# Kernel optimization log

Hardware: AMD Instinct MI355X
Metric: run time of the kernel (lower is better)

## Reference

```python
import jax, jax.numpy as jnp
import numpy as np
import math

B, T, D, NH, HD = 2, 1024, 768, 12, 64
V, L, E, CAP_F, H = 50257, 2, 8, 1.25, 2048
AUX_W, Z_W, THETA, EPS = 0.01, 0.001, 10000.0, 1e-5
N = B * T
CAP = int(math.ceil(N / E * CAP_F))  # 320


def setup_inputs():
    key = jax.random.key(0)
    ks = jax.random.split(key, 8)
    s = 0.02
    return dict(
        idx=jax.random.randint(ks[0], (B, T), 0, V),
        wte=jax.random.normal(ks[1], (V, D), jnp.float32) * s,
        wqkv=jax.random.normal(ks[2], (L, D, 3 * D), jnp.float32) * s,
        q_norm_w=jnp.ones((L, D), jnp.float32),
        k_norm_w=jnp.ones((L, D), jnp.float32),
        o_proj=jax.random.normal(ks[3], (L, D, D), jnp.float32) * s,
        ffn_norm_w=jnp.ones((L, D), jnp.float32),
        gate_w=jax.random.normal(ks[4], (L, D, E), jnp.float32) * s,
        w13=jax.random.normal(ks[5], (L, E, D, 2 * H), jnp.float32) * s,
        w2=jax.random.normal(ks[6], (L, E, H, D), jnp.float32) * s,
        ln_f_w=jnp.ones((D,), jnp.float32),
    )


def rmsnorm(x, w):
    return x * jax.lax.rsqrt(jnp.mean(x * x, axis=-1, keepdims=True) + EPS) * w


def rope(x, cos, sin):
    # x: (B, nh, T, HD) viewed as complex pairs on last dim
    xr = x.reshape(*x.shape[:-1], HD // 2, 2)
    x0, x1 = xr[..., 0], xr[..., 1]
    out = jnp.stack([x0 * cos - x1 * sin, x0 * sin + x1 * cos], axis=-1)
    return out.reshape(x.shape)


def moe(x, gate_w, w13, w2):
    # x: (B, T, D) -> Switch MoE (k=1) with capacity CAP and token drops
    x_flat = x.reshape(N, D).astype(jnp.float32)
    logits = x_flat @ gate_w  # (N, E) fp32
    probs = jax.nn.softmax(logits, axis=-1)
    top = jnp.argmax(logits, axis=-1)  # (N,)
    prob_mass = probs.mean(axis=0)
    fraction = jax.nn.one_hot(top, E, dtype=jnp.float32).mean(axis=0)
    balance_loss = jnp.sum(prob_mass * fraction) * AUX_W * E
    z = jax.nn.logsumexp(logits, axis=-1)
    z_loss = jnp.mean(z * z) * Z_W
    aux = balance_loss + z_loss

    sort_idx = jnp.argsort(top)  # stable
    sorted_assign = top[sort_idx]
    counts = jnp.bincount(sorted_assign, length=E)
    offsets = jnp.concatenate([jnp.zeros((1,), counts.dtype), jnp.cumsum(counts)])[:E]
    rank = jnp.arange(N) - offsets[sorted_assign]  # position within expert segment
    keep = rank < CAP
    x_perm = x_flat[sort_idx]
    slot = jnp.where(keep, rank, CAP)  # dropped -> overflow slot
    buf = jnp.zeros((E, CAP + 1, D), jnp.float32).at[sorted_assign, slot].set(x_perm)
    xb = buf[:, :CAP]  # (E, CAP, D)
    gu = jnp.einsum('ecd,edh->ech', xb, w13)  # (E, CAP, 2H)
    g, u = jnp.split(gu, 2, axis=-1)
    y = jnp.einsum('ech,ehd->ecd', jax.nn.silu(g) * u, w2)  # (E, CAP, D)
    out_perm = y[sorted_assign, jnp.minimum(rank, CAP - 1)] * keep[:, None]
    out_flat = jnp.zeros((N, D), jnp.float32).at[sort_idx].set(out_perm)
    return out_flat.reshape(B, T, D), aux, top.reshape(B, T), keep[jnp.argsort(sort_idx)].reshape(B, T)


def forward(idx, wte, wqkv, q_norm_w, k_norm_w, o_proj, ffn_norm_w, gate_w, w13, w2, ln_f_w):
    x = wte[idx]  # (B, T, D)
    freqs = 1.0 / (THETA ** (jnp.arange(0, HD, 2, dtype=jnp.float32) / HD))
    ang = jnp.outer(jnp.arange(T, dtype=jnp.float32), freqs)  # (T, HD//2)
    cos, sin = jnp.cos(ang)[None, None], jnp.sin(ang)[None, None]
    mask = jnp.where(jnp.tril(jnp.ones((T, T), bool)), 0.0, -jnp.inf)
    aux_total = jnp.float32(0.0)
    for l in range(L):
        qkv = x @ wqkv[l]
        q, k, v = jnp.split(qkv, 3, axis=-1)
        q = rmsnorm(q, q_norm_w[l])
        k = rmsnorm(k, k_norm_w[l])
        q = q.reshape(B, T, NH, HD).transpose(0, 2, 1, 3)
        k = k.reshape(B, T, NH, HD).transpose(0, 2, 1, 3)
        v = v.reshape(B, T, NH, HD).transpose(0, 2, 1, 3)
        q, k = rope(q, cos, sin), rope(k, cos, sin)
        scores = jnp.einsum('bhqd,bhkd->bhqk', q, k) / math.sqrt(HD) + mask
        attn = jax.nn.softmax(scores, axis=-1)
        y = jnp.einsum('bhqk,bhkd->bhqd', attn, v).transpose(0, 2, 1, 3).reshape(B, T, D)
        h = x + y @ o_proj[l]
        ffn_in = rmsnorm(h, ffn_norm_w[l])
        moe_out, aux, _, _ = moe(ffn_in, gate_w[l], w13[l], w2[l])
        aux_total = aux_total + aux
        x = h + moe_out
    x = rmsnorm(x, ln_f_w)
    logits = x @ wte.T  # tied lm_head
    return logits, aux_total


def reference(idx, wte, wqkv, q_norm_w, k_norm_w, o_proj, ffn_norm_w, gate_w, w13, w2, ln_f_w):
    return forward(idx, wte, wqkv, q_norm_w, k_norm_w, o_proj, ffn_norm_w, gate_w, w13, w2, ln_f_w)
```

## Files before the change

### kernel.cpp

```cpp
#include <hip/hip_runtime.h>

typedef __attribute__((ext_vector_type(8))) _Float16 half8;
typedef __attribute__((ext_vector_type(4))) float f32x4;

constexpr int Bc = 2, Tc = 1024, Dc = 768, NHc = 12, HDc = 64;
constexpr int Vc = 50257, Lc = 2, Ec = 8, Hc = 2048;
constexpr int Ntok = Bc * Tc;
constexpr int CAPc = 320, CAPPc = 384;
constexpr long long LOGITS_N = (long long)Bc * Tc * Vc;

typedef const __attribute__((address_space(1))) unsigned int* gas_t;
typedef __attribute__((address_space(3))) unsigned int* las_t;
__device__ __forceinline__ void gload16(const void* g, void* l) {
  __builtin_amdgcn_global_load_lds((gas_t)g, (las_t)l, 16, 0, 0);
}

__device__ __forceinline__ void splitf16(float a, unsigned short& h, unsigned short& l) {
  _Float16 hh = (_Float16)a;
  _Float16 ll = (_Float16)(a - (float)hh);
  h = __builtin_bit_cast(unsigned short, hh);
  l = __builtin_bit_cast(unsigned short, ll);
}
__device__ __forceinline__ unsigned short f16o(float a) {
  _Float16 hh = (_Float16)a;
  return __builtin_bit_cast(unsigned short, hh);
}


__global__ void zero_small(float* psum, float* z2) {
  int t = threadIdx.x;
  if (t < Lc * Ec) psum[t] = 0.f;
  if (t < Lc) z2[t] = 0.f;
}

__global__ void embed_k(const int* __restrict__ idx, const float* __restrict__ wte,
                        float* __restrict__ x, unsigned short* __restrict__ x16) {
  int n = blockIdx.x;
  long long v = idx[n];
  const float4* src = (const float4*)(wte + v * 768);
  float4* dst = (float4*)(x + (long long)n * 768);
  int t = threadIdx.x;
  if (t < 192) {
    float4 val = src[t];
    dst[t] = val;
    ushort4 h, l;
    splitf16(val.x, h.x, l.x); splitf16(val.y, h.y, l.y);
    splitf16(val.z, h.z, l.z); splitf16(val.w, h.w, l.w);
    unsigned short* d = x16 + (long long)n * 1536 + t * 4;
    *(ushort4*)d = h;
    *(ushort4*)(d + 768) = l;
  }
}

__global__ void f2h4(const float* __restrict__ in, unsigned short* __restrict__ out,
                     long long n4) {
  long long i = (long long)blockIdx.x * 256 + threadIdx.x;
  if (i >= n4) return;
  float4 v = ((const float4*)in)[i];
  ushort4 o;
  o.x = f16o(v.x); o.y = f16o(v.y); o.z = f16o(v.z); o.w = f16o(v.w);
  ((ushort4*)out)[i] = o;
}

template <int SP>
__global__ void __launch_bounds__(256) split2_wT(const float* __restrict__ src,
    unsigned short* __restrict__ dst, int K, int N, long long sS, long long sD) {
  __shared__ float t[32][33];
  int z = blockIdx.z;
  src += (long long)z * sS;
  dst += (long long)z * sD;
  int n0 = blockIdx.x * 32, k0 = blockIdx.y * 32;
  int tid = threadIdx.x;
  int r = tid >> 3, c4 = (tid & 7) * 4;
  float4 v = *(const float4*)(src + (long long)(k0 + r) * N + n0 + c4);
  t[r][c4 + 0] = v.x; t[r][c4 + 1] = v.y; t[r][c4 + 2] = v.z; t[r][c4 + 3] = v.w;
  __syncthreads();
  int n = tid >> 3, kq = (tid & 7) * 4;
  ushort4 h, l;
  splitf16(t[kq + 0][n], h.x, l.x);
  splitf16(t[kq + 1][n], h.y, l.y);
  splitf16(t[kq + 2][n], h.z, l.z);
  splitf16(t[kq + 3][n], h.w, l.w);
  const int lda = SP ? 2 * K : K;
  unsigned short* d = dst + (long long)(n0 + n) * lda + k0 + kq;
  *(ushort4*)d = h;
  if (SP) *(ushort4*)(d + K) = l;
}

__global__ void __launch_bounds__(256) rmsnorm_k(const float* in, int istride,
                                                 float* outp, int ostride,
                                                 const float* w) {
  long long n = blockIdx.x;
  const float* xr = in + n * istride;
  float* yr = outp + n * ostride;
  int tid = threadIdx.x;
  float s = 0.f;
  for (int i = tid; i < 768; i += 256) { float v = xr[i]; s += v * v; }
  #pragma unroll
  for (int o = 32; o; o >>= 1) s += __shfl_down(s, o);
  __shared__ float red[4];
  __shared__ float bs;
  if ((tid & 63) == 0) red[tid >> 6] = s;
  __syncthreads();
  if (tid == 0) bs = rsqrtf((red[0] + red[1] + red[2] + red[3]) / 768.0f + 1e-5f);
  __syncthreads();
  float sc = bs;
  for (int i = tid; i < 768; i += 256) yr[i] = xr[i] * sc * w[i];
}

__global__ void __launch_bounds__(256) rmsnorm_h(const float* in,
                                                 unsigned short* outp, const float* w) {
  long long n = blockIdx.x;
  const float* xr = in + n * 768;
  unsigned short* yr = outp + n * 768;
  int tid = threadIdx.x;
  float s = 0.f;
  for (int i = tid; i < 768; i += 256) { float v = xr[i]; s += v * v; }
  #pragma unroll
  for (int o = 32; o; o >>= 1) s += __shfl_down(s, o);
  __shared__ float red[4];
  __shared__ float bs;
  if ((tid & 63) == 0) red[tid >> 6] = s;
  __syncthreads();
  if (tid == 0) bs = rsqrtf((red[0] + red[1] + red[2] + red[3]) / 768.0f + 1e-5f);
  __syncthreads();
  float sc = bs;
  for (int i = tid; i < 768; i += 256) yr[i] = f16o(xr[i] * sc * w[i]);
}

__global__ void __launch_bounds__(256) qk_rope(const float* __restrict__ qkv,
    const float* __restrict__ qnw, const float* __restrict__ knw,
    unsigned short* __restrict__ qr, unsigned short* __restrict__ kr,
    unsigned short* __restrict__ vr) {
  int n = blockIdx.x;
  int t = n & 1023, b = n >> 10;
  const float* row = qkv + (long long)n * 2304;
  int tid = threadIdx.x;
  float sq = 0.f, sk = 0.f;
  for (int i = tid; i < 768; i += 256) {
    float q = row[i]; sq += q * q;
    float k = row[768 + i]; sk += k * k;
  }
  #pragma unroll
  for (int o = 32; o; o >>= 1) { sq += __shfl_down(sq, o); sk += __shfl_down(sk, o); }
  __shared__ float redq[4], redk[4];
  __shared__ float bq, bk;
  if ((tid & 63) == 0) { redq[tid >> 6] = sq; redk[tid >> 6] = sk; }
  __syncthreads();
  if (tid == 0) {
    bq = rsqrtf((redq[0] + redq[1] + redq[2] + redq[3]) / 768.0f + 1e-5f);
    bk = rsqrtf((redk[0] + redk[1] + redk[2] + redk[3]) / 768.0f + 1e-5f);
  }
  __syncthreads();
  float nq = bq, nk = bk;
  for (int i = tid; i < 384; i += 256) {
    int hh = i >> 5, j = i & 31;
    int c = hh * 64 + 2 * j;
    float ang = (float)t * powf(10000.0f, -((float)j * (1.0f / 32.0f)));
    float cs = cosf(ang), sn = sinf(ang);
    int z = b * 12 + hh;
    long long qb = ((long long)z * 1024 + t) * 128 + 2 * j;
    unsigned short h0, l0, h1, l1;
    float q0 = row[c] * nq * qnw[c], q1 = row[c + 1] * nq * qnw[c + 1];
    splitf16(q0 * cs - q1 * sn, h0, l0);
    splitf16(q0 * sn + q1 * cs, h1, l1);
    *(unsigned int*)&qr[qb] = (unsigned)h0 | ((unsigned)h1 << 16);
    *(unsigned int*)&qr[qb + 64] = (unsigned)l0 | ((unsigned)l1 << 16);
    float k0 = row[768 + c] * nk * knw[c], k1 = row[768 + c + 1] * nk * knw[c + 1];
    splitf16(k0 * cs - k1 * sn, h0, l0);
    splitf16(k0 * sn + k1 * cs, h1, l1);
    *(unsigned int*)&kr[qb] = (unsigned)h0 | ((unsigned)h1 << 16);
    *(unsigned int*)&kr[qb + 64] = (unsigned)l0 | ((unsigned)l1 << 16);
    splitf16(row[1536 + c], h0, l0);
    splitf16(row[1536 + c + 1], h1, l1);
    long long vb = ((long long)z * 64 + 2 * j) * 2048 + t;
    vr[vb] = h0; vr[vb + 1024] = l0;
    vr[vb + 2048] = h1; vr[vb + 3072] = l1;
  }
}

__global__ void __launch_bounds__(256) flash_attn(
    const unsigned short* __restrict__ qr, const unsigned short* __restrict__ kr,
    const unsigned short* __restrict__ vr, unsigned short* __restrict__ yout) {
  __shared__ __align__(16) unsigned short Ph[4][16][72];
  __shared__ __align__(16) unsigned short Pl[4][16][72];
  int bid = blockIdx.x;
  int z = bid >> 4;
  int qt = 15 - (bid & 15);
  int b = z / 12, h = z % 12;
  int q0 = qt * 64;
  int wave = threadIdx.x >> 6, lane = threadIdx.x & 63;
  int lr = lane & 15, lg = lane >> 4;
  int qw = q0 + wave * 16;
  half8 af[2][2];
  const unsigned short* qbase = qr + ((long long)z * 1024 + qw + lr) * 128;
  #pragma unroll
  for (int ks = 0; ks < 2; ++ks)
    #pragma unroll
    for (int p = 0; p < 2; ++p)
      af[ks][p] = *(const half8*)(qbase + p * 64 + ks * 32 + lg * 8);
  f32x4 accy[4];
  #pragma unroll
  for (int df = 0; df < 4; ++df) accy[df] = (f32x4){0.f, 0.f, 0.f, 0.f};
  float mrun[4] = {-3.4e38f, -3.4e38f, -3.4e38f, -3.4e38f};
  float srun[4] = {0.f, 0.f, 0.f, 0.f};
  for (int kt = 0; kt <= qt; ++kt) {
    int kv0 = kt * 64;
    f32x4 s[4];
    #pragma unroll
    for (int nf = 0; nf < 4; ++nf) s[nf] = (f32x4){0.f, 0.f, 0.f, 0.f};
    const unsigned short* kbase = kr + ((long long)z * 1024 + kv0 + lr) * 128;
    #pragma unroll
    for (int nf = 0; nf < 4; ++nf) {
      const unsigned short* kb = kbase + nf * 16 * 128;
      #pragma unroll
      for (int ks = 0; ks < 2; ++ks) {
        half8 bh = *(const half8*)(kb + ks * 32 + lg * 8);
        half8 bl = *(const half8*)(kb + 64 + ks * 32 + lg * 8);
        s[nf] = __builtin_amdgcn_mfma_f32_16x16x32_f16(af[ks][0], bh, s[nf], 0, 0, 0);
        s[nf] = __builtin_amdgcn_mfma_f32_16x16x32_f16(af[ks][1], bh, s[nf], 0, 0, 0);
        s[nf] = __builtin_amdgcn_mfma_f32_16x16x32_f16(af[ks][0], bl, s[nf], 0, 0, 0);
      }
    }
    bool diag = (kt == qt);
    #pragma unroll
    for (int nf = 0; nf < 4; ++nf)
      #pragma unroll
      for (int j = 0; j < 4; ++j) {
        float v = s[nf][j] * 0.125f;
        if (diag && (nf * 16 + lr > wave * 16 + lg * 4 + j)) v = -1e30f;
        s[nf][j] = v;
      }
    #pragma unroll
    for (int j = 0; j < 4; ++j) {
      float tm = fmaxf(fmaxf(s[0][j], s[1][j]), fmaxf(s[2][j], s[3][j]));
      #pragma unroll
      for (int o = 1; o < 16; o <<= 1) tm = fmaxf(tm, __shfl_xor(tm, o));
      float mnew = fmaxf(mrun[j], tm);
      float sc = expf(mrun[j] - mnew);
      float ts = 0.f;
      #pragma unroll
      for (int nf = 0; nf < 4; ++nf) {
        float p = expf(s[nf][j] - mnew);
        ts += p;
        unsigned short ph, pl;
        splitf16(p, ph, pl);
        Ph[wave][lg * 4 + j][nf * 16 + lr] = ph;
        Pl[wave][lg * 4 + j][nf * 16 + lr] = pl;
      }
      #pragma unroll
      for (int o = 1; o < 16; o <<= 1) ts += __shfl_xor(ts, o);
      srun[j] = srun[j] * sc + ts;
      mrun[j] = mnew;
      #pragma unroll
      for (int df = 0; df < 4; ++df) accy[df][j] *= sc;
    }
    #pragma unroll
    for (int ks2 = 0; ks2 < 2; ++ks2) {
      half8 aph = *(const half8*)&Ph[wave][lr][ks2 * 32 + lg * 8];
      half8 apl = *(const half8*)&Pl[wave][lr][ks2 * 32 + lg * 8];
      #pragma unroll
      for (int df = 0; df < 4; ++df) {
        const unsigned short* vb =
            vr + ((long long)z * 64 + df * 16 + lr) * 2048 + kv0 + ks2 * 32 + lg * 8;
        half8 bvh = *(const half8*)vb;
        half8 bvl = *(const half8*)(vb + 1024);
        accy[df] = __builtin_amdgcn_mfma_f32_16x16x32_f16(aph, bvh, accy[df], 0, 0, 0);
        accy[df] = __builtin_amdgcn_mfma_f32_16x16x32_f16(apl, bvh, accy[df], 0, 0, 0);
        accy[df] = __builtin_amdgcn_mfma_f32_16x16x32_f16(aph, bvl, accy[df], 0, 0, 0);
      }
    }
  }
  float inv[4];
  #pragma unroll
  for (int j = 0; j < 4; ++j) inv[j] = 1.0f / srun[j];
  #pragma unroll
  for (int df = 0; df < 4; ++df)
    #pragma unroll
    for (int j = 0; j < 4; ++j) {
      long long tok = (long long)b * 1024 + qw + lg * 4 + j;
      int col = h * 64 + df * 16 + lr;
      unsigned short hh, ll;
      splitf16(accy[df][j] * inv[j], hh, ll);
      yout[tok * 1536 + col] = hh;
      yout[tok * 1536 + 768 + col] = ll;
    }
}

__global__ void __launch_bounds__(256) gate_k(const float* __restrict__ xin,
    const float* __restrict__ gw, int* __restrict__ top,
    float* __restrict__ psum, float* __restrict__ z2) {
  __shared__ float gws[768 * 8];
  __shared__ float pacc[8];
  __shared__ float zacc;
  int tid = threadIdx.x;
  for (int i = tid; i < 768 * 8 / 4; i += 256) ((float4*)gws)[i] = ((const float4*)gw)[i];
  if (tid < 8) pacc[tid] = 0.f;
  if (tid == 0) zacc = 0.f;
  __syncthreads();
  int n = blockIdx.x * 256 + tid;
  const float4* xr4 = (const float4*)(xin + (long long)n * 768);
  float l[8] = {0, 0, 0, 0, 0, 0, 0, 0};
  for (int d4 = 0; d4 < 192; ++d4) {
    float4 xv = xr4[d4];
    const float* g = &gws[d4 * 32];
    #pragma unroll
    for (int e = 0; e < 8; ++e)
      l[e] += xv.x * g[e] + xv.y * g[8 + e] + xv.z * g[16 + e] + xv.w * g[24 + e];
  }
  float mx = l[0]; int bi = 0;
  #pragma unroll
  for (int e = 1; e < 8; ++e) if (l[e] > mx) { mx = l[e]; bi = e; }
  float p[8]; float se = 0.f;
  #pragma unroll
  for (int e = 0; e < 8; ++e) { p[e] = expf(l[e] - mx); se += p[e]; }
  float z = mx + logf(se);
  top[n] = bi;
  #pragma unroll
  for (int e = 0; e < 8; ++e) atomicAdd(&pacc[e], p[e] / se);
  atomicAdd(&zacc, z * z);
  __syncthreads();
  if (tid < 8) atomicAdd(&psum[tid], pacc[tid]);
  if (tid == 0) atomicAdd(z2, zacc);
}

__global__ void route_scan(const int* __restrict__ top, int* __restrict__ rank,
                           int* __restrict__ cnt) {
  int lane = threadIdx.x;
  int c[8] = {0, 0, 0, 0, 0, 0, 0, 0};
  unsigned long long below = (1ull << lane) - 1ull;
  for (int s = 0; s < Ntok / 64; ++s) {
    int n = s * 64 + lane;
    int e = top[n];
    int r = 0;
    #pragma unroll
    for (int q = 0; q < 8; ++q) {
      unsigned long long m = __ballot(e == q);
      if (e == q) r = c[q] + __popcll(m & below);
      c[q] += __popcll(m);
    }
    rank[n] = r;
  }
  #pragma unroll
  for (int q = 0; q < 8; ++q) if (lane == q) cnt[q] = c[q];
}

template <int SP>
__global__ void scatter_xb(const float* __restrict__ xin, const int* __restrict__ top,
                           const int* __restrict__ rank, unsigned short* __restrict__ xb) {
  int n = blockIdx.x;
  int r = rank[n];
  if (r >= CAPc) return;
  int e = top[n];
  int t = threadIdx.x;
  if (t >= 192) return;
  float4 v = ((const float4*)(xin + (long long)n * 768))[t];
  ushort4 h, l;
  splitf16(v.x, h.x, l.x); splitf16(v.y, h.y, l.y);
  splitf16(v.z, h.z, l.z); splitf16(v.w, h.w, l.w);
  const int lda = SP ? 1536 : 768;
  unsigned short* dst = xb + ((long long)e * CAPPc + r) * lda + t * 4;
  *(ushort4*)dst = h;
  if (SP) *(ushort4*)(dst + 768) = l;
}

template <int SP>
__global__ void __launch_bounds__(256) silu_k(const float* __restrict__ gu,
                                              unsigned short* __restrict__ act) {
  long long i = (long long)blockIdx.x * 256 + threadIdx.x;
  long long row = i >> 11;
  int h = (int)(i & 2047);
  float g = gu[row * 4096 + h];
  float u = gu[row * 4096 + 2048 + h];
  float a = g / (1.f + expf(-g)) * u;
  if (SP) {
    unsigned short hh, ll;
    splitf16(a, hh, ll);
    act[row * 4096 + h] = hh;
    act[row * 4096 + 2048 + h] = ll;
  } else {
    act[row * 2048 + h] = f16o(a);
  }
}

__global__ void gather_add(const float* __restrict__ h, const float* __restrict__ yexp,
                           const int* __restrict__ top, const int* __restrict__ rank,
                           float* __restrict__ xo, unsigned short* __restrict__ x16) {
  int n = blockIdx.x;
  int r = rank[n], e = top[n];
  bool kept = r < CAPc;
  int rc = kept ? r : (CAPc - 1);
  const float4* hs = (const float4*)(h + (long long)n * 768);
  const float4* ys = (const float4*)(yexp + ((long long)e * CAPPc + rc) * 768);
  float4* dst = (float4*)(xo + (long long)n * 768);
  int t = threadIdx.x;
  if (t < 192) {
    float4 v = hs[t];
    if (kept) { float4 y = ys[t]; v.x += y.x; v.y += y.y; v.z += y.z; v.w += y.w; }
    dst[t] = v;
    ushort4 hh, ll;
    splitf16(v.x, hh.x, ll.x); splitf16(v.y, hh.y, ll.y);
    splitf16(v.z, hh.z, ll.z); splitf16(v.w, hh.w, ll.w);
    unsigned short* d = x16 + (long long)n * 1536 + t * 4;
    *(ushort4*)d = hh;
    *(ushort4*)(d + 768) = ll;
  }
}

__global__ void aux_fin(const float* __restrict__ psum, const int* __restrict__ cnt,
                        const float* __restrict__ z2, float* __restrict__ outp) {
  if (threadIdx.x == 0) {
    float aux = 0.f;
    for (int l = 0; l < Lc; ++l) {
      float bl = 0.f;
      for (int e = 0; e < 8; ++e)
        bl += (psum[l * 8 + e] * (1.0f / 2048.0f)) * ((float)cnt[l * 8 + e] * (1.0f / 2048.0f));
      aux += bl * (0.01f * 8.0f) + (z2[l] * (1.0f / 2048.0f)) * 0.001f;
    }
    outp[0] = aux;
  }
}

template <int BN, int SPLIT, int ADD, int NTAIL>
__global__ void __launch_bounds__(256) gemm_h(
    const unsigned short* __restrict__ A, const unsigned short* __restrict__ Bt,
    float* __restrict__ C, const float* __restrict__ Add,
    int M, int N, int K, int ldc, int gx, int gy,
    long long sA, long long sB, int zdiv, long long sC1, long long sC2) {
  constexpr int FN = (BN == 128) ? 4 : 2;
  constexpr int APL = 128 * 32;
  constexpr int BPL = BN * 32;
  constexpr int BUF = 2 * APL + 2 * BPL;
  __shared__ __align__(16) unsigned short lds[2][BUF];
  int tot = gridDim.x;
  int lin = blockIdx.x;
  if ((tot & 7) == 0) lin = (lin & 7) * (tot >> 3) + (lin >> 3);
  int pz = lin / (gx * gy);
  int r2 = lin - pz * (gx * gy);
  const int m0 = (r2 % gx) * 128, n0 = (r2 / gx) * BN;
  A += (long long)pz * sA;
  Bt += (long long)pz * sB;
  const long long co = (long long)(pz / zdiv) * sC1 + (long long)(pz % zdiv) * sC2;
  const int lda = SPLIT ? 2 * K : K;
  const int NS = SPLIT ? K / 32 : K / 64;
  const int tid = threadIdx.x;
  const int lane = tid & 63, wave = tid >> 6;
  const int wm = (BN == 128) ? (wave >> 1) : (wave & 1);
  const int wn = (BN == 128) ? (wave & 1) : (wave >> 1);
  const int srow = tid >> 2, scol = (tid & 3) * 8;
  const unsigned short* Ar = A + (long long)(m0 + srow) * lda + scol;
  int br0 = n0 + srow;
  if (NTAIL) br0 = min(br0, N - 1);
  const unsigned short* Br = Bt + (long long)br0 * lda + scol;
  int br1 = n0 + srow + 64;
  if (NTAIL) br1 = min(br1, N - 1);
  const unsigned short* Br2 = Bt + (long long)br1 * lda + scol;

  auto STAGE = [&](int buf, int s) {
    const int kh = SPLIT ? s * 32 : s * 64;
    const int kl = SPLIT ? K + s * 32 : s * 64 + 32;
    unsigned short* L = lds[buf];
    gload16(Ar + kh, &L[wave * 512]);
    gload16(Ar + (long long)64 * lda + kh, &L[2048 + wave * 512]);
    gload16(Ar + kl, &L[APL + wave * 512]);
    gload16(Ar + (long long)64 * lda + kl, &L[APL + 2048 + wave * 512]);
    gload16(Br + kh, &L[2 * APL + wave * 512]);
    gload16(Br + kl, &L[2 * APL + BPL + wave * 512]);
    if (BN == 128) {
      gload16(Br2 + kh, &L[2 * APL + 2048 + wave * 512]);
      gload16(Br2 + kl, &L[2 * APL + BPL + 2048 + wave * 512]);
    }
  };

  f32x4 acc[4][FN];
  #pragma unroll
  for (int m = 0; m < 4; ++m)
    #pragma unroll
    for (int n = 0; n < FN; ++n) acc[m][n] = (f32x4){0.f, 0.f, 0.f, 0.f};

  STAGE(0, 0);
  int cur = 0;
  for (int s = 0; s < NS; ++s) {
    if (s + 1 < NS) {
      STAGE(cur ^ 1, s + 1);
      if constexpr (BN == 128)
        asm volatile("s_waitcnt vmcnt(8)" ::: "memory");
      else
        asm volatile("s_waitcnt vmcnt(6)" ::: "memory");
    } else {
      asm volatile("s_waitcnt vmcnt(0)" ::: "memory");
    }
    __builtin_amdgcn_sched_barrier(0);
    __builtin_amdgcn_s_barrier();
    const unsigned short* L = lds[cur];
    half8 bfh[FN], bfl[FN];
    #pragma unroll
    for (int n = 0; n < FN; ++n) {
      int bo = (wn * (FN * 16) + n * 16 + (lane & 15)) * 32 + (lane >> 4) * 8;
      bfh[n] = *(const half8*)&L[2 * APL + bo];
      bfl[n] = *(const half8*)&L[2 * APL + BPL + bo];
    }
    __builtin_amdgcn_s_setprio(1);
    #pragma unroll
    for (int m = 0; m < 4; ++m) {
      int ao = (wm * 64 + m * 16 + (lane & 15)) * 32 + (lane >> 4) * 8;
      half8 afh = *(const half8*)&L[ao];
      half8 afl = *(const half8*)&L[APL + ao];
      #pragma unroll
      for (int n = 0; n < FN; ++n) {
        acc[m][n] = __builtin_amdgcn_mfma_f32_16x16x32_f16(afh, bfh[n], acc[m][n], 0, 0, 0);
        if (SPLIT) {
          acc[m][n] = __builtin_amdgcn_mfma_f32_16x16x32_f16(afl, bfh[n], acc[m][n], 0, 0, 0);
          acc[m][n] = __builtin_amdgcn_mfma_f32_16x16x32_f16(afh, bfl[n], acc[m][n], 0, 0, 0);
        } else {
          acc[m][n] = __builtin_amdgcn_mfma_f32_16x16x32_f16(afl, bfl[n], acc[m][n], 0, 0, 0);
        }
      }
    }
    __builtin_amdgcn_s_setprio(0);
    __builtin_amdgcn_sched_barrier(0);
    __builtin_amdgcn_s_barrier();
    cur ^= 1;
  }
  #pragma unroll
  for (int m = 0; m < 4; ++m)
    #pragma unroll
    for (int n = 0; n < FN; ++n) {
      int col = n0 + wn * (FN * 16) + n * 16 + (lane & 15);
      if (!NTAIL || col < N) {
        #pragma unroll
        for (int j = 0; j < 4; ++j) {
          long long row = m0 + wm * 64 + m * 16 + (lane >> 4) * 4 + j;
          long long o = co + row * ldc + col;
          float v = acc[m][n][j];
          if (ADD) v += Add[o];
          C[o] = v;
        }
      }
    }
}


extern "C" void kernel_launch(void* const* d_in, const int* in_sizes, int n_in,
                              void* d_out, int out_size, void* d_ws, size_t ws_size,
                              hipStream_t stream) {
  (void)in_sizes; (void)n_in; (void)out_size; (void)ws_size;
  const int*   idx   = (const int*)d_in[0];
  const float* wte   = (const float*)d_in[1];
  const float* wqkv  = (const float*)d_in[2];
  const float* qnw   = (const float*)d_in[3];
  const float* knw   = (const float*)d_in[4];
  const float* oproj = (const float*)d_in[5];
  const float* ffnw  = (const float*)d_in[6];
  const float* gatew = (const float*)d_in[7];
  const float* w13   = (const float*)d_in[8];
  const float* w2p   = (const float*)d_in[9];
  const float* lnf   = (const float*)d_in[10];
  float* out = (float*)d_out;

  char* base = (char*)d_ws;
  size_t off = 0;
  auto alloc = [&](size_t bytes) -> char* {
    off = (off + 255) & ~(size_t)255;
    char* p = base + off; off += bytes; return p;
  };
  float* x     = (float*)alloc((size_t)Ntok * 768 * 4);
  float* qkv   = (float*)alloc((size_t)Ntok * 2304 * 4);
  float* hbuf  = (float*)alloc((size_t)Ntok * 768 * 4);
  float* ffn   = (float*)alloc((size_t)Ntok * 768 * 4);
  unsigned short* x16   = (unsigned short*)alloc((size_t)Ntok * 1536 * 2);
  unsigned short* yfl16 = (unsigned short*)alloc((size_t)Ntok * 1536 * 2);
  unsigned short* qr16  = (unsigned short*)alloc((size_t)24 * 1024 * 128 * 2);
  unsigned short* kr16  = (unsigned short*)alloc((size_t)24 * 1024 * 128 * 2);
  unsigned short* vr16  = (unsigned short*)alloc((size_t)24 * 64 * 2048 * 2);
  unsigned short* xb16  = (unsigned short*)alloc((size_t)Ec * CAPPc * 1536 * 2);
  unsigned short* wo16  = (unsigned short*)alloc((size_t)768 * 1536 * 2);
  unsigned short* xf16  = (unsigned short*)alloc((size_t)Ntok * 768 * 2);
  char* spb = alloc((size_t)24 * 1024 * 1024 * 4);
  float* gu   = (float*)spb;
  float* yexp = (float*)spb;
  unsigned short* act16 = (unsigned short*)(spb + 50331648);
  unsigned short* wq16  = (unsigned short*)(spb + 75497472);
  unsigned short* w13_16 = (unsigned short*)alloc((size_t)Ec * 4096 * 1536 * 2);
  unsigned short* wt16   = w13_16;
  unsigned short* w2_16  = (unsigned short*)alloc((size_t)Ec * 768 * 4096 * 2);
  int* top    = (int*)alloc(Ntok * 4);
  int* rankb  = (int*)alloc(Ntok * 4);
  int* cnt    = (int*)alloc(Lc * Ec * 4);
  float* psum = (float*)alloc(Lc * Ec * 4);
  float* z2   = (float*)alloc(Lc * 4);

  zero_small<<<1, 64, 0, stream>>>(psum, z2);
  embed_k<<<Ntok, 192, 0, stream>>>(idx, wte, x, x16);

  for (int l = 0; l < Lc; ++l) {
    split2_wT<1><<<dim3(72, 24, 1), 256, 0, stream>>>(wqkv + (size_t)l * 768 * 2304, wq16,
                                                      768, 2304, 0, 0);
    split2_wT<1><<<dim3(24, 24, 1), 256, 0, stream>>>(oproj + (size_t)l * 768 * 768, wo16,
                                                      768, 768, 0, 0);
    if (l == 0) {
      split2_wT<1><<<dim3(128, 24, 8), 256, 0, stream>>>(w13, w13_16,
          768, 4096, (long long)768 * 4096, (long long)4096 * 1536);
      split2_wT<1><<<dim3(24, 64, 8), 256, 0, stream>>>(w2p, w2_16,
          2048, 768, (long long)2048 * 768, (long long)768 * 4096);
    } else {
      split2_wT<0><<<dim3(128, 24, 8), 256, 0, stream>>>(w13 + (size_t)Ec * 768 * 4096, w13_16,
          768, 4096, (long long)768 * 4096, (long long)4096 * 768);
      split2_wT<0><<<dim3(24, 64, 8), 256, 0, stream>>>(w2p + (size_t)Ec * 2048 * 768, w2_16,
          2048, 768, (long long)2048 * 768, (long long)768 * 2048);
    }
    gemm_h<128, 1, 0, 0><<<288, 256, 0, stream>>>(
        x16, wq16, qkv, nullptr, 2048, 2304, 768, 2304, 16, 18, 0, 0, 1, 0, 0);
    qk_rope<<<Ntok, 256, 0, stream>>>(qkv, qnw + l * 768, knw + l * 768, qr16, kr16, vr16);
    flash_attn<<<384, 256, 0, stream>>>(qr16, kr16, vr16, yfl16);
    gemm_h<64, 1, 1, 0><<<192, 256, 0, stream>>>(
        yfl16, wo16, hbuf, x, 2048, 768, 768, 768, 16, 12, 0, 0, 1, 0, 0);
    rmsnorm_k<<<Ntok, 256, 0, stream>>>(hbuf, 768, ffn, 768, ffnw + l * 768);
    gate_k<<<Ntok / 256, 256, 0, stream>>>(ffn, gatew + (size_t)l * 768 * 8, top,
                                           psum + l * 8, z2 + l);
    route_scan<<<1, 64, 0, stream>>>(top, rankb, cnt + l * 8);
    if (l == 0) {
      scatter_xb<1><<<Ntok, 192, 0, stream>>>(ffn, top, rankb, xb16);
      gemm_h<128, 1, 0, 0><<<768, 256, 0, stream>>>(
          xb16, w13_16, gu, nullptr, 384, 4096, 768, 4096, 3, 32,
          (long long)384 * 1536, (long long)4096 * 1536, 1, (long long)384 * 4096, 0);
      silu_k<1><<<(Ec * CAPPc * Hc) / 256, 256, 0, stream>>>(gu, act16);
      gemm_h<64, 1, 0, 0><<<288, 256, 0, stream>>>(
          act16, w2_16, yexp, nullptr, 384, 768, 2048, 768, 3, 12,
          (long long)384 * 4096, (long long)768 * 4096, 1, (long long)384 * 768, 0);
    } else {
      scatter_xb<0><<<Ntok, 192, 0, stream>>>(ffn, top, rankb, xb16);
      gemm_h<128, 0, 0, 0><<<768, 256, 0, stream>>>(
          xb16, w13_16, gu, nullptr, 384, 4096, 768, 4096, 3, 32,
          (long long)384 * 768, (long long)4096 * 768, 1, (long long)384 * 4096, 0);
      silu_k<0><<<(Ec * CAPPc * Hc) / 256, 256, 0, stream>>>(gu, act16);
      gemm_h<64, 0, 0, 0><<<288, 256, 0, stream>>>(
          act16, w2_16, yexp, nullptr, 384, 768, 2048, 768, 3, 12,
          (long long)384 * 2048, (long long)768 * 2048, 1, (long long)384 * 768, 0);
    }
    gather_add<<<Ntok, 192, 0, stream>>>(hbuf, yexp, top, rankb, x, x16);
  }

  rmsnorm_h<<<Ntok, 256, 0, stream>>>(x, xf16, lnf);
  f2h4<<<(int)(((long long)Vc * 768 / 4 + 255) / 256), 256, 0, stream>>>(
      wte, wt16, (long long)Vc * 768 / 4);
  gemm_h<128, 0, 0, 1><<<6288, 256, 0, stream>>>(
      xf16, wt16, out, nullptr, 2048, Vc, 768, Vc, 16, 393, 0, 0, 1, 0, 0);
  aux_fin<<<1, 64, 0, stream>>>(psum, cnt, z2, out + LOGITS_N);
}
```

Measured before the change: 1.286 ms.

## Add dedicated triple-buffered 256x128 MFMA GEMM for the tied lm_head logits

Replaces the generic gemm_h call for the final vocabulary projection with a specialized kernel. It uses 256x128 tiles, 512 threads, three LDS stages fed by async global-to-LDS loads, an XOR-swizzled LDS layout and an XCD-aware block remap. The aim is to overlap loads with MFMA work and reuse more data per tile in the largest GEMM. The cost is higher LDS use per block (about 144 KB), which limits occupancy. Row indices outside N are clamped, so the wasted loads in the tail tile stay in bounds.

```diff
diff --git a/kernel.cpp b/kernel.cpp
--- a/kernel.cpp
+++ b/kernel.cpp
@@ -540,6 +540,102 @@
     }
 }
 
+__global__ void __launch_bounds__(512) gemm_logits(
+    const unsigned short* __restrict__ A, const unsigned short* __restrict__ Bt,
+    float* __restrict__ C, int M, int N, int K, int ldc, int gx) {
+  constexpr int BUFS = 24576;
+  constexpr int BOFF = 16384;
+  __shared__ __align__(16) unsigned short lds[3 * BUFS];
+  int tot = gridDim.x;
+  int lin = blockIdx.x;
+  if ((tot & 7) == 0) lin = (lin & 7) * (tot >> 3) + (lin >> 3);
+  const int m0 = (lin % gx) * 256, n0 = (lin / gx) * 128;
+  const int tid = threadIdx.x;
+  const int lane = tid & 63;
+  const int wm = (tid >> 6) >> 1, wn = (tid >> 6) & 1;
+  const int NS = K / 64;
+
+  auto STAGE = [&](int buf, int t) {
+    const int k0 = t * 64;
+    unsigned short* L = lds + buf * BUFS;
+    #pragma unroll
+    for (int i = 0; i < 4; ++i) {
+      int idx = tid + i * 512;
+      int row = idx >> 3, blk = idx & 7;
+      gload16(A + (long long)(m0 + row) * K + k0 + ((blk ^ (row & 7)) << 3),
+              L + idx * 8);
+    }
+    #pragma unroll
+    for (int i = 0; i < 2; ++i) {
+      int idx = tid + i * 512;
+      int row = idx >> 3, blk = idx & 7;
+      int br = min(n0 + row, N - 1);
+      gload16(Bt + (long long)br * K + k0 + ((blk ^ (row & 7)) << 3),
+              L + BOFF + idx * 8);
+    }
+  };
+
+  f32x4 acc[4][4];
+  #pragma unroll
+  for (int mf = 0; mf < 4; ++mf)
+    #pragma unroll
+    for (int nf = 0; nf < 4; ++nf) acc[mf][nf] = (f32x4){0.f, 0.f, 0.f, 0.f};
+
+  STAGE(0, 0); STAGE(1, 1); STAGE(2, 2);
+  for (int s = 0; s < NS; ++s) {
+    if (s + 3 <= NS)      asm volatile("s_waitcnt vmcnt(12)" ::: "memory");
+    else if (s + 2 <= NS) asm volatile("s_waitcnt vmcnt(6)" ::: "memory");
+    else                  asm volatile("s_waitcnt vmcnt(0)" ::: "memory");
+    __builtin_amdgcn_sched_barrier(0);
+    __builtin_amdgcn_s_barrier();
+    const unsigned short* L = lds + (s % 3) * BUFS;
+    half8 a[4][2], b[4][2];
+    #pragma unroll
+    for (int mf = 0; mf < 4; ++mf)
+      #pragma unroll
+      for (int ks = 0; ks < 2; ++ks) {
+        int row = wm * 64 + mf * 16 + (lane & 15);
+        int blk = (ks * 4 + (lane >> 4)) ^ (row & 7);
+        a[mf][ks] = *(const half8*)(L + row * 64 + blk * 8);
+      }
+    #pragma unroll
+    for (int nf = 0; nf < 4; ++nf)
+      #pragma unroll
+      for (int ks = 0; ks < 2; ++ks) {
+        int row = wn * 64 + nf * 16 + (lane & 15);
+        int blk = (ks * 4 + (lane >> 4)) ^ (row & 7);
+        b[nf][ks] = *(const half8*)(L + BOFF + row * 64 + blk * 8);
+      }
+    asm volatile("s_waitcnt lgkmcnt(0)" ::: "memory");
+    __builtin_amdgcn_sched_barrier(0);
+    __builtin_amdgcn_s_barrier();
+    if (s + 3 < NS) STAGE((s + 3) % 3, s + 3);
+    __builtin_amdgcn_s_setprio(1);
+    #pragma unroll
+    for (int ks = 0; ks < 2; ++ks)
+      #pragma unroll
+      for (int mf = 0; mf < 4; ++mf)
+        #pragma unroll
+        for (int nf = 0; nf < 4; ++nf)
+          acc[mf][nf] = __builtin_amdgcn_mfma_f32_16x16x32_f16(a[mf][ks], b[nf][ks],
+                                                               acc[mf][nf], 0, 0, 0);
+    __builtin_amdgcn_s_setprio(0);
+  }
+  #pragma unroll
+  for (int mf = 0; mf < 4; ++mf)
+    #pragma unroll
+    for (int nf = 0; nf < 4; ++nf) {
+      int col = n0 + wn * 64 + nf * 16 + (lane & 15);
+      if (col < N) {
+        #pragma unroll
+        for (int j = 0; j < 4; ++j) {
+          long long row = m0 + wm * 64 + mf * 16 + (lane >> 4) * 4 + j;
+          C[row * (long long)ldc + col] = acc[mf][nf][j];
+        }
+      }
+    }
+}
+
 
 extern "C" void kernel_launch(void* const* d_in, const int* in_sizes, int n_in,
                               void* d_out, int out_size, void* d_ws, size_t ws_size,
@@ -644,7 +740,6 @@
   rmsnorm_h<<<Ntok, 256, 0, stream>>>(x, xf16, lnf);
   f2h4<<<(int)(((long long)Vc * 768 / 4 + 255) / 256), 256, 0, stream>>>(
       wte, wt16, (long long)Vc * 768 / 4);
-  gemm_h<128, 0, 0, 1><<<6288, 256, 0, stream>>>(
-      xf16, wt16, out, nullptr, 2048, Vc, 768, Vc, 16, 393, 0, 0, 1, 0, 0);
+  gemm_logits<<<8 * 393, 512, 0, stream>>>(xf16, wt16, out, 2048, Vc, 768, Vc, 8);
   aux_fin<<<1, 64, 0, stream>>>(psum, cnt, z2, out + LOGITS_N);
 }
```

Measured after the change: 1.304 ms. About the same (+1.4%).
